# Kernel optimization log

Hardware: AMD Instinct MI355X
Metric: run time of the kernel (lower is better)

## Reference

```python
import jax, jax.numpy as jnp
import numpy as np

HEADS, HEAD_DIM, WS = 12, 32, 7
DISP = WS // 2


def _shift_masks(ws, d):
    # upper/lower mask: blocks crossing the wrapped boundary in the row direction
    ul = np.zeros((ws * ws, ws * ws), np.float32)
    ul[-d * ws:, :-d * ws] = -np.inf
    ul[:-d * ws, -d * ws:] = -np.inf
    # left/right mask: columns crossing the wrapped boundary
    lr = np.zeros((ws, ws, ws, ws), np.float32)
    lr[:, -d:, :, :-d] = -np.inf
    lr[:, :-d, :, -d:] = -np.inf
    lr = lr.reshape(ws * ws, ws * ws)
    return jnp.asarray(ul), jnp.asarray(lr)


def _rel_indices(ws):
    idx = np.arange(ws)
    coords = np.stack(np.meshgrid(idx, idx, indexing='ij'), -1).reshape(-1, 2)  # [[x,y] row-major]
    rel = coords[None, :, :] - coords[:, None, :] + ws - 1  # (ws^2, ws^2, 2)
    return jnp.asarray(rel)


def setup_inputs() -> dict:
    key = jax.random.key(0)
    ks = jax.random.split(key, 7)
    b, H, W, dim = 16, 56, 56, 384
    inner = HEADS * HEAD_DIM
    x = jax.random.normal(ks[0], (b, H, W, dim), jnp.float32)
    w_qkv = jax.random.normal(ks[1], (dim, 3 * inner), jnp.float32) * (dim ** -0.5)
    pos_embedding = jax.random.normal(ks[2], (2 * WS - 1, 2 * WS - 1), jnp.float32) * 0.02
    w_out = jax.random.normal(ks[3], (inner, dim), jnp.float32) * (inner ** -0.5)
    b_out = jnp.zeros((dim,), jnp.float32)
    w_post = jax.random.normal(ks[4], (dim, dim), jnp.float32) * (dim ** -0.5)
    b_post = jnp.zeros((dim,), jnp.float32)
    return {"x": x, "w_qkv": w_qkv, "pos_embedding": pos_embedding,
            "w_out": w_out, "b_out": b_out, "w_post": w_post, "b_post": b_post}


def reference(x, w_qkv, pos_embedding, w_out, b_out, w_post, b_post):
    b, H, W, dim = x.shape
    nw_h, nw_w = H // WS, W // WS
    scale = HEAD_DIM ** -0.5

    # cyclic shift
    x = jnp.roll(x, shift=(-DISP, -DISP), axis=(1, 2))

    # qkv projection (no bias), window partition -> (3, b, h, nw, ws^2, d)
    qkv = (x @ w_qkv).reshape(b, nw_h, WS, nw_w, WS, 3, HEADS, HEAD_DIM)
    qkv = qkv.transpose(5, 0, 6, 1, 3, 2, 4, 7).reshape(3, b, HEADS, nw_h * nw_w, WS * WS, HEAD_DIM)
    q, k, v = qkv[0], qkv[1], qkv[2]

    dots = jnp.einsum('bhwid,bhwjd->bhwij', q, k) * scale

    # relative position bias gather
    rel = _rel_indices(WS)
    dots = dots + pos_embedding[rel[..., 0], rel[..., 1]]

    # shifted-window masks
    ul, lr = _shift_masks(WS, DISP)
    dots = dots.at[:, :, -nw_w:].add(ul)
    dots = dots.at[:, :, nw_w - 1::nw_w].add(lr)

    attn = jax.nn.softmax(dots, axis=-1)
    out = jnp.einsum('bhwij,bhwjd->bhwid', attn, v)

    # merge windows back -> (b, H, W, inner)
    out = out.reshape(b, HEADS, nw_h, nw_w, WS, WS, HEAD_DIM)
    out = out.transpose(0, 2, 4, 3, 5, 1, 6).reshape(b, H, W, HEADS * HEAD_DIM)

    out = out @ w_out + b_out
    out = out @ w_post + b_post  # post_drop is identity in eval
    out = jnp.roll(out, shift=(DISP, DISP), axis=(1, 2))
    return out
```

## Files before the change

### kernel.cpp

```cpp
#include <hip/hip_runtime.h>
#include <hip/hip_bf16.h>
#include <stdint.h>

typedef __bf16 bf16_t;
typedef bf16_t bf16x8 __attribute__((ext_vector_type(8)));
typedef bf16_t bf16x4 __attribute__((ext_vector_type(4)));
typedef float f32x4 __attribute__((ext_vector_type(4)));

#define BATCH 16
#define HH    56
#define DIMK  384
#define M_TOT (BATCH*HH*HH)
#define SCALE 0.17677669529663687f

__device__ __forceinline__ void async_load16(const bf16_t* g, const bf16_t* l) {
  __builtin_amdgcn_global_load_lds((const __attribute__((address_space(1))) void*)g,
                                   (__attribute__((address_space(3))) void*)l,
                                   16, 0, 0);
}

template<int CTRL>
__device__ __forceinline__ float dpp_ror(float x) {
  return __int_as_float(__builtin_amdgcn_mov_dpp(__float_as_int(x), CTRL, 0xf, 0xf, false));
}
__device__ __forceinline__ float rowmax16(float v) {
  v = fmaxf(v, dpp_ror<0x121>(v));
  v = fmaxf(v, dpp_ror<0x122>(v));
  v = fmaxf(v, dpp_ror<0x124>(v));
  v = fmaxf(v, dpp_ror<0x128>(v));
  return v;
}
__device__ __forceinline__ float rowsum16(float v) {
  v += dpp_ror<0x121>(v);
  v += dpp_ror<0x122>(v);
  v += dpp_ror<0x124>(v);
  v += dpp_ror<0x128>(v);
  return v;
}

__global__ void k_zero(float* __restrict__ p, int n) {
  int i = blockIdx.x * 256 + threadIdx.x;
  if (i < n) p[i] = 0.f;
}

__global__ void k_transpose(const float* __restrict__ w, bf16_t* __restrict__ wT) {
  int idx = blockIdx.x * 256 + threadIdx.x;
  if (idx >= 1152 * 384) return;
  int n = idx / 384, k = idx - n * 384;
  wT[idx] = (bf16_t)w[k * 1152 + n];
}

__global__ void k_comb(const float* __restrict__ w_out, const float* __restrict__ b_out,
                       const float* __restrict__ w_post, const float* __restrict__ b_post,
                       bf16_t* __restrict__ wcombT, float* __restrict__ bcomb) {
  __shared__ float col[384];
  const int n = blockIdx.x, t = threadIdx.x;
  for (int j = t; j < 384; j += 256) col[j] = w_post[j * 384 + n];
  __syncthreads();
  for (int k = t; k < 384; k += 256) {
    float acc = 0.f;
    for (int j = 0; j < 384; ++j) acc += w_out[k * 384 + j] * col[j];
    wcombT[n * 384 + k] = (bf16_t)acc;
  }
  if (t == 0) {
    float acc = b_post[n];
    for (int j = 0; j < 384; ++j) acc += b_out[j] * col[j];
    bcomb[n] = acc;
  }
}

__global__ void k_bias(const float* __restrict__ pos, float* __restrict__ biasC) {
  int idx = blockIdx.x * 256 + threadIdx.x;
  if (idx >= 4 * 16 * 64 * 4) return;
  int reg = idx & 3, lane = (idx >> 2) & 63, tile = (idx >> 8) & 15, cls = idx >> 12;
  int mt = tile >> 2, nt = tile & 3, lc = lane & 15, quad = lane >> 4;
  int m = mt * 16 + quad * 4 + reg, n = nt * 16 + lc;
  float v = -1e32f;
  if (m < 49 && n < 49) {
    int ty = m / 7, tx = m % 7, jy = n / 7, jx = n % 7;
    bool dead = ((cls & 1) && ((m >= 28) != (n >= 28))) ||
                ((cls & 2) && ((tx >= 4) != (jx >= 4)));
    v = dead ? -1e32f : pos[(jy - ty + 6) * 13 + (jx - tx + 6)] * (1.0f / SCALE);
  }
  biasC[idx] = v;
}

__global__ void k_convroll(const float* __restrict__ x, bf16_t* __restrict__ xb) {
  int idx = blockIdx.x * 256 + threadIdx.x;
  if (idx >= M_TOT * 48) return;
  int row = idx / 48, c = idx - row * 48;
  int bb = row / 3136, rem = row - bb * 3136, i = rem / 56, j = rem - i * 56;
  int si = i + 3; if (si >= 56) si -= 56;
  int sj = j + 3; if (sj >= 56) sj -= 56;
  const float* src = x + ((size_t)(bb * 3136 + si * 56 + sj)) * 384 + c * 8;
  f32x4 v0 = *(const f32x4*)src;
  f32x4 v1 = *(const f32x4*)(src + 4);
  bf16x8 o;
#pragma unroll
  for (int u = 0; u < 4; ++u) { o[u] = (bf16_t)v0[u]; o[4 + u] = (bf16_t)v1[u]; }
  *(bf16x8*)(xb + (size_t)row * 384 + c * 8) = o;
}

template<int MODE>
__global__ __launch_bounds__(256)
void k_gemm(const bf16_t* __restrict__ A, const bf16_t* __restrict__ B,
            void* __restrict__ Cv, const float* __restrict__ bias,
            int Ndim, int Kdim, int lda) {
  __shared__ __align__(16) bf16_t As[2][128 * 32];
  __shared__ __align__(16) bf16_t Bs[2][128 * 32];
  const int tid  = threadIdx.x;
  const int wave = tid >> 6;
  const int lane = tid & 63;
  const int wr = wave >> 1, wc = wave & 1;

  const int gx   = gridDim.x;
  const int nwg  = gx * gridDim.y;
  const int flat = blockIdx.y * gx + blockIdx.x;
  const int qch  = nwg >> 3;
  const int nf   = (flat & 7) * qch + (flat >> 3);
  const int bx   = nf % gx;
  const int by   = nf / gx;

  const int row0 = by * 128;
  const int col0 = bx * 128;

  const bf16_t* aptr[2];
  const bf16_t* bptr[2];
  int lin[2];
#pragma unroll
  for (int c = 0; c < 2; ++c) {
    int linear = c * 256 + tid;
    lin[c] = linear;
    int r  = linear >> 2;
    int kc = linear & 3;
    aptr[c] = A + (size_t)(row0 + r) * lda + kc * 8;
    bptr[c] = B + (size_t)(col0 + r) * Kdim + kc * 8;
  }

  f32x4 acc[4][4] = {};
  const int lr = lane >> 4;
  const int lc = lane & 15;
  unsigned aoff[4], boff[4];
#pragma unroll
  for (int mi = 0; mi < 4; ++mi) aoff[mi] = (unsigned)((wr * 64 + mi * 16 + lc) * 32 + lr * 8);
#pragma unroll
  for (int ni = 0; ni < 4; ++ni) boff[ni] = (unsigned)((wc * 64 + ni * 16 + lc) * 32 + lr * 8);

  const int kiters = Kdim >> 5;

  {
    async_load16(aptr[0], As[0] + lin[0] * 8);
    async_load16(aptr[1], As[0] + lin[1] * 8);
    async_load16(bptr[0], Bs[0] + lin[0] * 8);
    async_load16(bptr[1], Bs[0] + lin[1] * 8);
  }

  for (int kt = 0; kt < kiters; ++kt) {
    const int cur = kt & 1;
    __syncthreads();
    if (kt + 1 < kiters) {
      const int koff = (kt + 1) * 32;
      async_load16(aptr[0] + koff, As[cur ^ 1] + lin[0] * 8);
      async_load16(aptr[1] + koff, As[cur ^ 1] + lin[1] * 8);
      async_load16(bptr[0] + koff, Bs[cur ^ 1] + lin[0] * 8);
      async_load16(bptr[1] + koff, Bs[cur ^ 1] + lin[1] * 8);
    }
    bf16x8 af[4], bfr[4];
#pragma unroll
    for (int mi = 0; mi < 4; ++mi) af[mi]  = *(const bf16x8*)(As[cur] + aoff[mi]);
#pragma unroll
    for (int ni = 0; ni < 4; ++ni) bfr[ni] = *(const bf16x8*)(Bs[cur] + boff[ni]);
#pragma unroll
    for (int mi = 0; mi < 4; ++mi)
#pragma unroll
      for (int ni = 0; ni < 4; ++ni)
        acc[mi][ni] = __builtin_amdgcn_mfma_f32_16x16x32_bf16(af[mi], bfr[ni], acc[mi][ni], 0, 0, 0);
  }

#pragma unroll
  for (int mi = 0; mi < 4; ++mi) {
#pragma unroll
    for (int rr = 0; rr < 4; ++rr) {
      int grow = row0 + wr * 64 + mi * 16 + lr * 4 + rr;
      size_t orow;
      if (MODE == 1) {
        int bb  = grow / 3136;
        int rem = grow - bb * 3136;
        int i = rem / 56;
        int j = rem - i * 56;
        int si = i + 3; if (si >= 56) si -= 56;
        int sj = j + 3; if (sj >= 56) sj -= 56;
        orow = (size_t)(bb * 3136 + si * 56 + sj);
      } else {
        orow = (size_t)grow;
      }
#pragma unroll
      for (int ni = 0; ni < 4; ++ni) {
        int gcol = col0 + wc * 64 + ni * 16 + lc;
        float v = acc[mi][ni][rr];
        if (MODE == 1) {
          ((float*)Cv)[orow * (size_t)Ndim + gcol] = v + bias[gcol];
        } else {
          ((bf16_t*)Cv)[orow * (size_t)Ndim + gcol] = (bf16_t)v;
        }
      }
    }
  }
}

__global__ __launch_bounds__(256)
void k_attn(const float* __restrict__ biasC, bf16_t* __restrict__ qkv) {
  __shared__ __align__(16) bf16_t Ps[4 * 64 * 72];
  const int tid = threadIdx.x, wid = tid >> 6, lane = tid & 63;
  const int p = blockIdx.x * 4 + wid;
  const int b = p / 768, rem = p - b * 768;
  const int head = rem >> 6, w = rem & 63;
  const int wy = w >> 3, wx = w & 7;
  const int cls = ((wy == 7) ? 1 : 0) | ((wx == 7) ? 2 : 0);
  const int lc = lane & 15, quad = lane >> 4;
  const size_t wbase = ((size_t)b * 3136 + (size_t)wy * 7 * 56 + (size_t)wx * 7) * 1152
                       + head * 32;

  auto rowoff = [&](int m) -> size_t {
    int ty = m / 7, tx = m - ty * 7;
    return wbase + (size_t)(ty * 56 + tx) * 1152;
  };

  bf16x8 qf[4], kf[4];
#pragma unroll
  for (int t = 0; t < 4; ++t) {
    int m = t * 16 + lc; if (m > 48) m = 48;
    const bf16_t* r = qkv + rowoff(m);
    qf[t] = *(const bf16x8*)(r + quad * 8);
    kf[t] = *(const bf16x8*)(r + 384 + quad * 8);
  }

  bf16x8 vf[2][2];
#pragma unroll
  for (int kc = 0; kc < 2; ++kc)
#pragma unroll
    for (int u = 0; u < 8; ++u) {
      int n = kc * 32 + quad * 8 + u; if (n > 48) n = 48;
      const bf16_t* r = qkv + rowoff(n) + 768 + lc;
      vf[kc][0][u] = r[0];
      vf[kc][1][u] = r[16];
    }

  f32x4 acc[4][4];
  const float* bp = biasC + cls * 4096 + lane * 4;
#pragma unroll
  for (int mt = 0; mt < 4; ++mt)
#pragma unroll
    for (int nt = 0; nt < 4; ++nt)
      acc[mt][nt] = *(const f32x4*)(bp + (mt * 4 + nt) * 256);
#pragma unroll
  for (int mt = 0; mt < 4; ++mt)
#pragma unroll
    for (int nt = 0; nt < 4; ++nt)
      acc[mt][nt] = __builtin_amdgcn_mfma_f32_16x16x32_bf16(qf[mt], kf[nt], acc[mt][nt], 0, 0, 0);

  float l[4][4];
#pragma unroll
  for (int mt = 0; mt < 4; ++mt)
#pragma unroll
    for (int reg = 0; reg < 4; ++reg) {
      float mx = fmaxf(fmaxf(acc[mt][0][reg], acc[mt][1][reg]),
                       fmaxf(acc[mt][2][reg], acc[mt][3][reg]));
      mx = rowmax16(mx);
      float s = 0.f;
#pragma unroll
      for (int nt = 0; nt < 4; ++nt) {
        float pe = __expf((acc[mt][nt][reg] - mx) * SCALE);
        acc[mt][nt][reg] = pe;
        s += pe;
      }
      l[mt][reg] = rowsum16(s);
    }

  bf16_t* P = Ps + wid * (64 * 72);
#pragma unroll
  for (int mt = 0; mt < 4; ++mt)
#pragma unroll
    for (int nt = 0; nt < 4; ++nt)
#pragma unroll
      for (int reg = 0; reg < 4; ++reg)
        P[(mt * 16 + quad * 4 + reg) * 72 + nt * 16 + lc] = (bf16_t)acc[mt][nt][reg];

  f32x4 oacc[4][2] = {};
#pragma unroll
  for (int mt = 0; mt < 4; ++mt) {
    bf16x8 pf0 = *(const bf16x8*)(P + (mt * 16 + lc) * 72 + quad * 8);
    bf16x8 pf1 = *(const bf16x8*)(P + (mt * 16 + lc) * 72 + 32 + quad * 8);
#pragma unroll
    for (int dt = 0; dt < 2; ++dt) {
      oacc[mt][dt] = __builtin_amdgcn_mfma_f32_16x16x32_bf16(pf0, vf[0][dt], oacc[mt][dt], 0, 0, 0);
      oacc[mt][dt] = __builtin_amdgcn_mfma_f32_16x16x32_bf16(pf1, vf[1][dt], oacc[mt][dt], 0, 0, 0);
    }
  }

#pragma unroll
  for (int mt = 0; mt < 4; ++mt)
#pragma unroll
    for (int reg = 0; reg < 4; ++reg) {
      int m = mt * 16 + quad * 4 + reg;
      if (m < 49) {
        float rl = __builtin_amdgcn_rcpf(l[mt][reg]);
        bf16_t* r = qkv + rowoff(m);
        r[lc]      = (bf16_t)(oacc[mt][0][reg] * rl);
        r[16 + lc] = (bf16_t)(oacc[mt][1][reg] * rl);
      }
    }
}

extern "C" void kernel_launch(void* const* d_in, const int* in_sizes, int n_in,
                              void* d_out, int out_size, void* d_ws, size_t ws_size,
                              hipStream_t stream) {
  const float* x      = (const float*)d_in[0];
  const float* w_qkv  = (const float*)d_in[1];
  const float* pos    = (const float*)d_in[2];
  const float* w_out  = (const float*)d_in[3];
  const float* b_out  = (const float*)d_in[4];
  const float* w_post = (const float*)d_in[5];
  const float* b_post = (const float*)d_in[6];
  float* out = (float*)d_out;

  const size_t SZ_QKV  = (size_t)M_TOT * 1152 * 2;
  const size_t SZ_WT   = (size_t)1152 * 384 * 2;
  const size_t SZ_WC   = (size_t)384 * 384 * 2;
  const size_t SZ_BC   = 384 * 4;
  const size_t SZ_BIAS = (size_t)4 * 16 * 64 * 4 * 4;
  const size_t NEEDED  = SZ_QKV + SZ_WT + SZ_WC + SZ_BC + SZ_BIAS;

  if (ws_size < NEEDED) {
    k_zero<<<(out_size + 255) / 256, 256, 0, stream>>>(out, out_size);
    return;
  }

  char* ws = (char*)d_ws;
  bf16_t* qkv   = (bf16_t*)ws;
  bf16_t* wT    = (bf16_t*)(ws + SZ_QKV);
  bf16_t* wcT   = (bf16_t*)(ws + SZ_QKV + SZ_WT);
  float*  bc    = (float*)(ws + SZ_QKV + SZ_WT + SZ_WC);
  float*  biasC = (float*)(ws + SZ_QKV + SZ_WT + SZ_WC + SZ_BC);
  bf16_t* xb    = (bf16_t*)d_out;

  k_transpose<<<1728, 256, 0, stream>>>(w_qkv, wT);
  k_comb<<<384, 256, 0, stream>>>(w_out, b_out, w_post, b_post, wcT, bc);
  k_bias<<<64, 256, 0, stream>>>(pos, biasC);
  k_convroll<<<(M_TOT * 48 + 255) / 256, 256, 0, stream>>>(x, xb);
  k_gemm<0><<<dim3(9, 392), 256, 0, stream>>>(xb, wT, qkv, nullptr, 1152, DIMK, DIMK);
  k_attn<<<3072, 256, 0, stream>>>(biasC, qkv);
  k_gemm<1><<<dim3(3, 392), 256, 0, stream>>>(qkv, wcT, out, bc, 384, DIMK, 1152);
}
```

Measured before the change: 318.0 us.

## Double GEMM K-tile to 64 with XOR-swizzled LDS layout

The GEMM K tile grows from 32 to 64, so each main-loop iteration does twice the MFMA work per barrier and there are half as many iterations and syncs. The LDS tile is stored with an XOR swizzle on the 16-byte column chunk (kc ^ row&7), applied through the global source address so the async LDS writes stay linear while fragment reads avoid bank conflicts. LDS use doubles to 64 KB per block, which may lower occupancy, and fragment registers double.

```diff
diff --git a/kernel.cpp b/kernel.cpp
--- a/kernel.cpp
+++ b/kernel.cpp
@@ -106,8 +106,8 @@
 void k_gemm(const bf16_t* __restrict__ A, const bf16_t* __restrict__ B,
             void* __restrict__ Cv, const float* __restrict__ bias,
             int Ndim, int Kdim, int lda) {
-  __shared__ __align__(16) bf16_t As[2][128 * 32];
-  __shared__ __align__(16) bf16_t Bs[2][128 * 32];
+  __shared__ __align__(16) bf16_t As[2][128 * 64];
+  __shared__ __align__(16) bf16_t Bs[2][128 * 64];
   const int tid  = threadIdx.x;
   const int wave = tid >> 6;
   const int lane = tid & 63;
@@ -124,57 +124,69 @@
   const int row0 = by * 128;
   const int col0 = bx * 128;
 
-  const bf16_t* aptr[2];
-  const bf16_t* bptr[2];
-  int lin[2];
-#pragma unroll
-  for (int c = 0; c < 2; ++c) {
+  const bf16_t* aptr[4];
+  const bf16_t* bptr[4];
+  int dst[4];
+#pragma unroll
+  for (int c = 0; c < 4; ++c) {
     int linear = c * 256 + tid;
-    lin[c] = linear;
-    int r  = linear >> 2;
-    int kc = linear & 3;
-    aptr[c] = A + (size_t)(row0 + r) * lda + kc * 8;
-    bptr[c] = B + (size_t)(col0 + r) * Kdim + kc * 8;
+    int r  = linear >> 3;
+    int kc = linear & 7;
+    int gk = kc ^ (r & 7);
+    dst[c] = linear * 8;
+    aptr[c] = A + (size_t)(row0 + r) * lda + gk * 8;
+    bptr[c] = B + (size_t)(col0 + r) * Kdim + gk * 8;
   }
 
   f32x4 acc[4][4] = {};
   const int lr = lane >> 4;
   const int lc = lane & 15;
-  unsigned aoff[4], boff[4];
-#pragma unroll
-  for (int mi = 0; mi < 4; ++mi) aoff[mi] = (unsigned)((wr * 64 + mi * 16 + lc) * 32 + lr * 8);
-#pragma unroll
-  for (int ni = 0; ni < 4; ++ni) boff[ni] = (unsigned)((wc * 64 + ni * 16 + lc) * 32 + lr * 8);
-
-  const int kiters = Kdim >> 5;
-
-  {
-    async_load16(aptr[0], As[0] + lin[0] * 8);
-    async_load16(aptr[1], As[0] + lin[1] * 8);
-    async_load16(bptr[0], Bs[0] + lin[0] * 8);
-    async_load16(bptr[1], Bs[0] + lin[1] * 8);
+  unsigned aoff[4][2], boff[4][2];
+#pragma unroll
+  for (int mi = 0; mi < 4; ++mi)
+#pragma unroll
+    for (int kh = 0; kh < 2; ++kh) {
+      int arow = wr * 64 + mi * 16 + lc;
+      int brow = wc * 64 + mi * 16 + lc;
+      int sc   = (kh * 4 + lr) ^ (lc & 7);
+      aoff[mi][kh] = (unsigned)(arow * 64 + sc * 8);
+      boff[mi][kh] = (unsigned)(brow * 64 + sc * 8);
+    }
+
+  const int kiters = Kdim >> 6;
+
+#pragma unroll
+  for (int c = 0; c < 4; ++c) {
+    async_load16(aptr[c], As[0] + dst[c]);
+    async_load16(bptr[c], Bs[0] + dst[c]);
   }
 
   for (int kt = 0; kt < kiters; ++kt) {
     const int cur = kt & 1;
     __syncthreads();
     if (kt + 1 < kiters) {
-      const int koff = (kt + 1) * 32;
-      async_load16(aptr[0] + koff, As[cur ^ 1] + lin[0] * 8);
-      async_load16(aptr[1] + koff, As[cur ^ 1] + lin[1] * 8);
-      async_load16(bptr[0] + koff, Bs[cur ^ 1] + lin[0] * 8);
-      async_load16(bptr[1] + koff, Bs[cur ^ 1] + lin[1] * 8);
-    }
-    bf16x8 af[4], bfr[4];
-#pragma unroll
-    for (int mi = 0; mi < 4; ++mi) af[mi]  = *(const bf16x8*)(As[cur] + aoff[mi]);
-#pragma unroll
-    for (int ni = 0; ni < 4; ++ni) bfr[ni] = *(const bf16x8*)(Bs[cur] + boff[ni]);
+      const int koff = (kt + 1) * 64;
+#pragma unroll
+      for (int c = 0; c < 4; ++c) {
+        async_load16(aptr[c] + koff, As[cur ^ 1] + dst[c]);
+        async_load16(bptr[c] + koff, Bs[cur ^ 1] + dst[c]);
+      }
+    }
+    bf16x8 af[4][2], bfr[4][2];
 #pragma unroll
     for (int mi = 0; mi < 4; ++mi)
 #pragma unroll
-      for (int ni = 0; ni < 4; ++ni)
-        acc[mi][ni] = __builtin_amdgcn_mfma_f32_16x16x32_bf16(af[mi], bfr[ni], acc[mi][ni], 0, 0, 0);
+      for (int kh = 0; kh < 2; ++kh) {
+        af[mi][kh]  = *(const bf16x8*)(As[cur] + aoff[mi][kh]);
+        bfr[mi][kh] = *(const bf16x8*)(Bs[cur] + boff[mi][kh]);
+      }
+#pragma unroll
+    for (int kh = 0; kh < 2; ++kh)
+#pragma unroll
+      for (int mi = 0; mi < 4; ++mi)
+#pragma unroll
+        for (int ni = 0; ni < 4; ++ni)
+          acc[mi][ni] = __builtin_amdgcn_mfma_f32_16x16x32_bf16(af[mi][kh], bfr[ni][kh], acc[mi][ni], 0, 0, 0);
   }
 
 #pragma unroll
```

Result: no change. 313.6 us (-1.4%).

## Use four-stage LDS ring with prefetch distance two and XOR-swizzled tiles

Applied to the files above, without the earlier changes.

The GEMM kernel's shared-memory buffers grow from two to four stages, and global-to-LDS async loads are issued two K-tiles ahead. Explicit vmcnt waits plus a raw s_barrier replace the per-iteration __syncthreads, so more memory latency can overlap with MFMA work. The K-chunk of each row is also XOR-swizzled on both the load and read side to cut LDS bank conflicts on the fragment reads. The cost is four times the LDS footprint, which may lower occupancy. The hand-written waitcnt and barrier logic must also stay correct with respect to buffer reuse.

```diff
diff --git a/kernel.cpp b/kernel.cpp
--- a/kernel.cpp
+++ b/kernel.cpp
@@ -106,8 +106,8 @@
 void k_gemm(const bf16_t* __restrict__ A, const bf16_t* __restrict__ B,
             void* __restrict__ Cv, const float* __restrict__ bias,
             int Ndim, int Kdim, int lda) {
-  __shared__ __align__(16) bf16_t As[2][128 * 32];
-  __shared__ __align__(16) bf16_t Bs[2][128 * 32];
+  __shared__ __align__(16) bf16_t As[4][128 * 32];
+  __shared__ __align__(16) bf16_t Bs[4][128 * 32];
   const int tid  = threadIdx.x;
   const int wave = tid >> 6;
   const int lane = tid & 63;
@@ -126,45 +126,59 @@
 
   const bf16_t* aptr[2];
   const bf16_t* bptr[2];
-  int lin[2];
+  int dst[2];
 #pragma unroll
   for (int c = 0; c < 2; ++c) {
     int linear = c * 256 + tid;
-    lin[c] = linear;
     int r  = linear >> 2;
     int kc = linear & 3;
-    aptr[c] = A + (size_t)(row0 + r) * lda + kc * 8;
-    bptr[c] = B + (size_t)(col0 + r) * Kdim + kc * 8;
+    int gk = kc ^ ((r >> 1) & 3);
+    dst[c] = linear * 8;
+    aptr[c] = A + (size_t)(row0 + r) * lda + gk * 8;
+    bptr[c] = B + (size_t)(col0 + r) * Kdim + gk * 8;
   }
 
   f32x4 acc[4][4] = {};
   const int lr = lane >> 4;
   const int lc = lane & 15;
   unsigned aoff[4], boff[4];
-#pragma unroll
-  for (int mi = 0; mi < 4; ++mi) aoff[mi] = (unsigned)((wr * 64 + mi * 16 + lc) * 32 + lr * 8);
-#pragma unroll
-  for (int ni = 0; ni < 4; ++ni) boff[ni] = (unsigned)((wc * 64 + ni * 16 + lc) * 32 + lr * 8);
+  const int scx = lr ^ ((lc >> 1) & 3);
+#pragma unroll
+  for (int mi = 0; mi < 4; ++mi) aoff[mi] = (unsigned)((wr * 64 + mi * 16 + lc) * 32 + scx * 8);
+#pragma unroll
+  for (int ni = 0; ni < 4; ++ni) boff[ni] = (unsigned)((wc * 64 + ni * 16 + lc) * 32 + scx * 8);
 
   const int kiters = Kdim >> 5;
 
-  {
-    async_load16(aptr[0], As[0] + lin[0] * 8);
-    async_load16(aptr[1], As[0] + lin[1] * 8);
-    async_load16(bptr[0], Bs[0] + lin[0] * 8);
-    async_load16(bptr[1], Bs[0] + lin[1] * 8);
+#pragma unroll
+  for (int c = 0; c < 2; ++c) {
+    async_load16(aptr[c], As[0] + dst[c]);
+    async_load16(bptr[c], Bs[0] + dst[c]);
+  }
+#pragma unroll
+  for (int c = 0; c < 2; ++c) {
+    async_load16(aptr[c] + 32, As[1] + dst[c]);
+    async_load16(bptr[c] + 32, Bs[1] + dst[c]);
   }
 
   for (int kt = 0; kt < kiters; ++kt) {
-    const int cur = kt & 1;
-    __syncthreads();
-    if (kt + 1 < kiters) {
-      const int koff = (kt + 1) * 32;
-      async_load16(aptr[0] + koff, As[cur ^ 1] + lin[0] * 8);
-      async_load16(aptr[1] + koff, As[cur ^ 1] + lin[1] * 8);
-      async_load16(bptr[0] + koff, Bs[cur ^ 1] + lin[0] * 8);
-      async_load16(bptr[1] + koff, Bs[cur ^ 1] + lin[1] * 8);
-    }
+    const int cur = kt & 3;
+    if (kt + 2 < kiters) {
+      const int koff = (kt + 2) * 32;
+      const int nb = (kt + 2) & 3;
+#pragma unroll
+      for (int c = 0; c < 2; ++c) {
+        async_load16(aptr[c] + koff, As[nb] + dst[c]);
+        async_load16(bptr[c] + koff, Bs[nb] + dst[c]);
+      }
+      asm volatile("s_waitcnt vmcnt(8)" ::: "memory");
+    } else if (kt + 2 == kiters) {
+      asm volatile("s_waitcnt vmcnt(4)" ::: "memory");
+    } else {
+      asm volatile("s_waitcnt vmcnt(0)" ::: "memory");
+    }
+    asm volatile("s_barrier" ::: "memory");
+
     bf16x8 af[4], bfr[4];
 #pragma unroll
     for (int mi = 0; mi < 4; ++mi) af[mi]  = *(const bf16x8*)(As[cur] + aoff[mi]);
```

After: 322.5 us. Within noise of the previous version (+1.4%).
